# Optimization experiments

Hardware: AMD Instinct MI355X
Metric: run time of the kernel (lower is better)

Reference implementation:

```python
import jax, jax.numpy as jnp
import numpy as np

N_NODES = 50000
N_REL = 4
N_EDGES = 250000
IN_F, HID_F, OUT_F = 512, 512, 256


def setup_inputs() -> dict:
    key = jax.random.key(0)
    ks = jax.random.split(key, 9)
    x = jax.random.normal(ks[0], (N_NODES, IN_F), dtype=jnp.float32)
    edge_src = jax.random.randint(ks[1], (N_REL, N_EDGES), 0, N_NODES, dtype=jnp.int64)
    edge_dst = jax.random.randint(ks[2], (N_REL, N_EDGES), 0, N_NODES, dtype=jnp.int64)
    s1 = 1.0 / np.sqrt(IN_F)
    s2 = 1.0 / np.sqrt(HID_F)
    Wself1 = jax.random.normal(ks[3], (N_REL, IN_F, HID_F), dtype=jnp.float32) * s1
    Wneigh1 = jax.random.normal(ks[4], (N_REL, IN_F, HID_F), dtype=jnp.float32) * s1
    b1 = jnp.zeros((N_REL, HID_F), dtype=jnp.float32)
    Wself2 = jax.random.normal(ks[5], (N_REL, HID_F, OUT_F), dtype=jnp.float32) * s2
    Wneigh2 = jax.random.normal(ks[6], (N_REL, HID_F, OUT_F), dtype=jnp.float32) * s2
    b2 = jnp.zeros((N_REL, OUT_F), dtype=jnp.float32)
    return {"x": x, "Wself1": Wself1, "Wneigh1": Wneigh1, "b1": b1,
            "Wself2": Wself2, "Wneigh2": Wneigh2, "b2": b2,
            "edge_src": edge_src, "edge_dst": edge_dst}


def _hetero_sage_layer(h, Wself, Wneigh, b, edge_src, edge_dst):
    """HeteroGraphConv(sum) over per-relation SAGEConv(mean) layers.

    DGL SAGEConv(mean): out_r = h @ W_self_r + mean_in_neigh(h) @ W_neigh_r + b_r;
    zero-in-degree nodes get a zero neighbor term (divide by max(deg,1)).
    """
    n = h.shape[0]
    out = jnp.zeros((n, Wself.shape[-1]), dtype=h.dtype)
    for r in range(Wself.shape[0]):  # small fixed number of relations
        src, dst = edge_src[r], edge_dst[r]
        deg = jax.ops.segment_sum(jnp.ones(src.shape, dtype=h.dtype), dst, num_segments=n)
        neigh_sum = jax.ops.segment_sum(h[src], dst, num_segments=n)  # [n, d]
        neigh = neigh_sum / jnp.maximum(deg, 1.0)[:, None]
        out = out + h @ Wself[r] + neigh @ Wneigh[r] + b[r]
    return out


def reference(x, Wself1, Wneigh1, b1, Wself2, Wneigh2, b2, edge_src, edge_dst):
    h = _hetero_sage_layer(x, Wself1, Wneigh1, b1, edge_src, edge_dst)
    h = jax.nn.relu(h)
    return _hetero_sage_layer(h, Wself2, Wneigh2, b2, edge_src, edge_dst)
```

## Files before the change

kernel.cpp:

```cpp
#include <hip/hip_runtime.h>
#include <stdint.h>

#define NNODES 50000
#define NREL 4
#define NEDGES 250000
#define INF 512
#define HIDF 512
#define OUTF 256
#define KCAT 2560
#define SCANB 49

typedef unsigned short u16;
typedef u16 u16x8 __attribute__((ext_vector_type(8)));
typedef __bf16 bf16x8 __attribute__((ext_vector_type(8)));
typedef float f32x4 __attribute__((ext_vector_type(4)));

__device__ __forceinline__ float bf2f(u16 b) {
    unsigned u = ((unsigned)b) << 16;
    return __builtin_bit_cast(float, u);
}
__device__ __forceinline__ u16 f2bf(float f) {
    unsigned u = __builtin_bit_cast(unsigned, f);
    u = (u + 0x7fffu + ((u >> 16) & 1u)) >> 16;
    return (u16)u;
}

#define GLOAD_LDS16(gsrc, ldst)                                                  \
    __builtin_amdgcn_global_load_lds(                                            \
        (__attribute__((address_space(1))) void*)(gsrc),                         \
        (__attribute__((address_space(3))) void*)(ldst), 16, 0, 0)


__global__ void cast_bf16_kernel(const float* __restrict__ in, u16* __restrict__ out, long total) {
    long i = ((long)blockIdx.x * blockDim.x + threadIdx.x) * 8;
    long stride = (long)gridDim.x * blockDim.x * 8;
    for (; i + 7 < total; i += stride) {
        float4 v0 = *(const float4*)(in + i);
        float4 v1 = *(const float4*)(in + i + 4);
        u16x8 o;
        o[0] = f2bf(v0.x); o[1] = f2bf(v0.y); o[2] = f2bf(v0.z); o[3] = f2bf(v0.w);
        o[4] = f2bf(v1.x); o[5] = f2bf(v1.y); o[6] = f2bf(v1.z); o[7] = f2bf(v1.w);
        *(u16x8*)(out + i) = o;
    }
}

__global__ __launch_bounds__(256) void prep_w_kernel(
    const float* __restrict__ Ws1, const float* __restrict__ Wn1,
    const float* __restrict__ Ws2, const float* __restrict__ Wn2,
    u16* __restrict__ WT1, u16* __restrict__ WT2) {
    __shared__ float tile[64][65];
    int bid = blockIdx.x;
    const float* Wself; const float* Wneigh; u16* WT;
    int N, s, kt, nt;
    if (bid < 320) {
        N = HIDF; WT = WT1; Wself = Ws1; Wneigh = Wn1;
        s = bid >> 6; int r = bid & 63; kt = r >> 3; nt = r & 7;
    } else {
        int b = bid - 320;
        N = OUTF; WT = WT2; Wself = Ws2; Wneigh = Wn2;
        s = b >> 5; int r = b & 31; kt = r >> 2; nt = r & 3;
    }
    int l = threadIdx.x & 63, wv = threadIdx.x >> 6;
    int n0 = nt * 64 + l;
    for (int i = 0; i < 16; ++i) {
        int kl = wv + i * 4;
        int k = kt * 64 + kl;
        float v;
        if (s == 0) {
            v = Wself[(size_t)k * N + n0] + Wself[((size_t)512 + k) * N + n0] +
                Wself[((size_t)1024 + k) * N + n0] + Wself[((size_t)1536 + k) * N + n0];
        } else {
            v = Wneigh[((size_t)(s - 1) * 512 + k) * N + n0];
        }
        tile[kl][l] = v;
    }
    __syncthreads();
    for (int i = 0; i < 16; ++i) {
        int nl = wv + i * 4;
        WT[(size_t)(nt * 64 + nl) * KCAT + s * 512 + kt * 64 + l] = f2bf(tile[l][nl]);
    }
}

__global__ void prep_bias_kernel(const float* __restrict__ b1, const float* __restrict__ b2,
                                 float* __restrict__ b1s, float* __restrict__ b2s) {
    int t = threadIdx.x;
    if (t < HIDF) b1s[t] = b1[t] + b1[HIDF + t] + b1[2 * HIDF + t] + b1[3 * HIDF + t];
    if (t < OUTF) b2s[t] = b2[t] + b2[OUTF + t] + b2[2 * OUTF + t] + b2[3 * OUTF + t];
}


__global__ void hist_kernel(const int* __restrict__ dst, int* __restrict__ deg) {
    int r = blockIdx.y;
    int i = blockIdx.x * blockDim.x + threadIdx.x;
    if (i < NEDGES) atomicAdd(&deg[r * NNODES + dst[r * NEDGES + i]], 1);
}

__global__ __launch_bounds__(1024) void scan1_kernel(const int* __restrict__ deg,
                                                     int* __restrict__ rp, int* __restrict__ bsum) {
    int rel = blockIdx.x / SCANB, blk = blockIdx.x % SCANB;
    int i = blk * 1024 + threadIdx.x;
    int v = (i < NNODES) ? deg[rel * NNODES + i] : 0;
    __shared__ int wsum[16];
    int lane = threadIdx.x & 63, wid = threadIdx.x >> 6;
    int x = v;
#pragma unroll
    for (int off = 1; off < 64; off <<= 1) {
        int o = __shfl_up(x, off);
        if (lane >= off) x += o;
    }
    if (lane == 63) wsum[wid] = x;
    __syncthreads();
    if (wid == 0) {
        int s = (lane < 16) ? wsum[lane] : 0;
#pragma unroll
        for (int off = 1; off < 16; off <<= 1) {
            int o = __shfl_up(s, off);
            if (lane >= off) s += o;
        }
        if (lane < 16) wsum[lane] = s;
    }
    __syncthreads();
    int excl = (wid > 0 ? wsum[wid - 1] : 0) + x - v;
    if (i < NNODES) rp[rel * (NNODES + 1) + i] = excl;
    if (threadIdx.x == 1023) bsum[blockIdx.x] = excl + v;
}

__global__ void scan2_kernel(const int* __restrict__ bsum, int* __restrict__ bofs) {
    int r = threadIdx.x >> 6, lane = threadIdx.x & 63;
    int v = (lane < SCANB) ? bsum[r * SCANB + lane] : 0;
    int x = v;
#pragma unroll
    for (int off = 1; off < 64; off <<= 1) {
        int o = __shfl_up(x, off);
        if (lane >= off) x += o;
    }
    if (lane < SCANB) bofs[r * SCANB + lane] = x - v;
}

__global__ __launch_bounds__(1024) void scan3_kernel(int* __restrict__ rp, int* __restrict__ cur,
                                                     const int* __restrict__ bofs) {
    int rel = blockIdx.x / SCANB, blk = blockIdx.x % SCANB;
    int i = blk * 1024 + threadIdx.x;
    if (i < NNODES) {
        int v = rp[rel * (NNODES + 1) + i] + bofs[rel * SCANB + blk];
        rp[rel * (NNODES + 1) + i] = v;
        cur[rel * NNODES + i] = v;
        if (i == 0) rp[rel * (NNODES + 1) + NNODES] = NEDGES;
    }
}

__global__ void fill_kernel(const int* __restrict__ esrc, const int* __restrict__ edst,
                            int* __restrict__ cur, int* __restrict__ col) {
    int r = blockIdx.y;
    int i = blockIdx.x * blockDim.x + threadIdx.x;
    if (i < NEDGES) {
        int d = edst[r * NEDGES + i];
        int pos = atomicAdd(&cur[r * NNODES + d], 1);
        col[r * NEDGES + pos] = esrc[r * NEDGES + i];
    }
}


__global__ __launch_bounds__(256) void aggregate_kernel(const u16* __restrict__ src,
                                                        const int* __restrict__ rp,
                                                        const int* __restrict__ col,
                                                        u16* __restrict__ out) {
    int node = blockIdx.x * 4 + (threadIdx.x >> 6);
    int rel = blockIdx.y;
    if (node >= NNODES) return;
    const int* r = rp + rel * (NNODES + 1);
    const int* cl = col + rel * NEDGES;
    int l = threadIdx.x & 63;
    int p0 = r[node], p1 = r[node + 1];
    int d = p1 - p0;
    float scale = (d > 0) ? 1.0f / (float)d : 1.0f;
    float acc[8] = {0.f, 0.f, 0.f, 0.f, 0.f, 0.f, 0.f, 0.f};
    const u16* srcl = src + l * 8;
    for (int base = 0; base < d; base += 64) {
        int ci = p0 + base + l;
        int myc = cl[ci < p1 ? ci : (p1 - 1)];
        int lim = d - base;
        if (lim > 64) lim = 64;
        for (int e = 0; e < lim; e += 8) {
            int idx[8]; float wgt[8];
#pragma unroll
            for (int j = 0; j < 8; ++j) {
                int ee = e + j;
                int lane = (ee < lim) ? ee : e;
                idx[j] = __builtin_amdgcn_readlane(myc, lane);
                wgt[j] = (ee < lim) ? scale : 0.0f;
            }
            u16x8 v[8];
#pragma unroll
            for (int j = 0; j < 8; ++j) v[j] = *(const u16x8*)(srcl + (size_t)idx[j] * 512);
#pragma unroll
            for (int j = 0; j < 8; ++j)
#pragma unroll
                for (int f = 0; f < 8; ++f) acc[f] += wgt[j] * bf2f(v[j][f]);
        }
    }
    u16x8 o;
#pragma unroll
    for (int j = 0; j < 8; ++j) o[j] = f2bf(acc[j]);
    *(u16x8*)(out + ((size_t)rel * NNODES + node) * 512 + l * 8) = o;
}


template <int N, int OUTMODE>
__global__ __launch_bounds__(256, 4) void gemm_kernel(
    const u16* __restrict__ A0, const u16* __restrict__ A1, const u16* __restrict__ A2,
    const u16* __restrict__ A3, const u16* __restrict__ A4, const u16* __restrict__ WT,
    const float* __restrict__ bias, void* __restrict__ outp, int M) {
    __shared__ u16 ldsA[128 * 64];
    __shared__ u16 ldsB[128 * 64];
    const int t = threadIdx.x;
    const int w = t >> 6, l = t & 63;
    const int wr = w >> 1, wc = w & 1;

    constexpr int ncol = N >> 7;
    const int nwg = gridDim.x * gridDim.y;
    const int orig = blockIdx.y * gridDim.x + blockIdx.x;
    const int q = nwg >> 3, rr = nwg & 7, xcd = orig & 7, loc = orig >> 3;
    const int v = (xcd < rr) ? xcd * (q + 1) + loc : rr * (q + 1) + (xcd - rr) * q + loc;
    const int rowBase = (v / ncol) * 128;
    const int colBase = (v % ncol) * 128;

    f32x4 acc[4][4] = {};

    const u16* const As[5] = {A0, A1, A2, A3, A4};
    const int sr = t >> 3;
    const int gp = t & 7;
    const int lr = l & 15, lg = l >> 4;

#pragma unroll
    for (int s = 0; s < 5; ++s) {
        const u16* __restrict__ Asrc = As[s];
        for (int ts = 0; ts < 8; ++ts) {
            const int klocal = ts * 64;
            const int kglob = s * 512 + klocal;
#pragma unroll
            for (int c = 0; c < 4; ++c) {
                int r = c * 32 + sr;
                int gl = gp ^ (r & 7);
                int grow = rowBase + r;
                if (grow > M - 1) grow = M - 1;
                const u16* gsrc = Asrc + (size_t)grow * 512 + klocal + gl * 8;
                GLOAD_LDS16(gsrc, ldsA + (c * 2048 + w * 512));
            }
#pragma unroll
            for (int c = 0; c < 4; ++c) {
                int r = c * 32 + sr;
                int gl = gp ^ (r & 7);
                const u16* gsrc = WT + (size_t)(colBase + r) * KCAT + kglob + gl * 8;
                GLOAD_LDS16(gsrc, ldsB + (c * 2048 + w * 512));
            }
            __syncthreads();
#pragma unroll
            for (int kh = 0; kh < 2; ++kh) {
                bf16x8 av[4], bv[4];
#pragma unroll
                for (int m = 0; m < 4; ++m) {
                    int r = wr * 64 + m * 16 + lr;
                    int g = (kh * 4 + lg) ^ (r & 7);
                    av[m] = *(const bf16x8*)((const char*)ldsA + r * 128 + g * 16);
                }
#pragma unroll
                for (int n = 0; n < 4; ++n) {
                    int r = wc * 64 + n * 16 + lr;
                    int g = (kh * 4 + lg) ^ (r & 7);
                    bv[n] = *(const bf16x8*)((const char*)ldsB + r * 128 + g * 16);
                }
#pragma unroll
                for (int m = 0; m < 4; ++m)
#pragma unroll
                    for (int n = 0; n < 4; ++n)
                        acc[m][n] =
                            __builtin_amdgcn_mfma_f32_16x16x32_bf16(av[m], bv[n], acc[m][n], 0, 0, 0);
            }
            __syncthreads();
        }
    }

    const int lq = l >> 4;
#pragma unroll
    for (int m = 0; m < 4; ++m) {
#pragma unroll
        for (int n = 0; n < 4; ++n) {
#pragma unroll
            for (int j = 0; j < 4; ++j) {
                int row = rowBase + wr * 64 + m * 16 + lq * 4 + j;
                int colc = colBase + wc * 64 + n * 16 + lr;
                if (row < M) {
                    float vv = acc[m][n][j] + bias[colc];
                    if (OUTMODE == 0) {
                        vv = vv > 0.f ? vv : 0.f;
                        ((u16*)outp)[(size_t)row * N + colc] = f2bf(vv);
                    } else {
                        ((float*)outp)[(size_t)row * N + colc] = vv;
                    }
                }
            }
        }
    }
}


extern "C" void kernel_launch(void* const* d_in, const int* in_sizes, int n_in,
                              void* d_out, int out_size, void* d_ws, size_t ws_size,
                              hipStream_t stream) {
    const float* x = (const float*)d_in[0];
    const float* Wself1 = (const float*)d_in[1];
    const float* Wneigh1 = (const float*)d_in[2];
    const float* b1 = (const float*)d_in[3];
    const float* Wself2 = (const float*)d_in[4];
    const float* Wneigh2 = (const float*)d_in[5];
    const float* b2 = (const float*)d_in[6];
    const int* esrc = (const int*)d_in[7];
    const int* edst = (const int*)d_in[8];

    char* ws = (char*)d_ws;
    size_t off = 0;
    auto alloc = [&](size_t bytes) {
        char* p = ws + off;
        off += (bytes + 255) & ~(size_t)255;
        return p;
    };
    const size_t plane = (size_t)NNODES * 512;
    u16* xB = (u16*)alloc(plane * 2);
    u16* mB = (u16*)alloc(NREL * plane * 2);
    u16* h1B = (u16*)alloc(plane * 2);
    u16* WT1 = (u16*)alloc((size_t)HIDF * KCAT * 2);
    u16* WT2 = (u16*)alloc((size_t)OUTF * KCAT * 2);
    float* b1s = (float*)alloc(HIDF * 4);
    float* b2s = (float*)alloc(OUTF * 4);
    int* deg = (int*)alloc((size_t)NREL * NNODES * 4);
    int* rp = (int*)alloc((size_t)NREL * (NNODES + 1) * 4);
    int* cur = (int*)alloc((size_t)NREL * NNODES * 4);
    int* col = (int*)alloc((size_t)NREL * NEDGES * 4);
    int* bsum = (int*)alloc((size_t)NREL * SCANB * 4);
    int* bofs = (int*)alloc((size_t)NREL * SCANB * 4);

    hipMemsetAsync(deg, 0, (size_t)NREL * NNODES * 4, stream);
    cast_bf16_kernel<<<12500, 256, 0, stream>>>(x, xB, (long)NNODES * INF);
    prep_w_kernel<<<480, 256, 0, stream>>>(Wself1, Wneigh1, Wself2, Wneigh2, WT1, WT2);
    prep_bias_kernel<<<1, 512, 0, stream>>>(b1, b2, b1s, b2s);
    hist_kernel<<<dim3(977, 4), 256, 0, stream>>>(edst, deg);
    scan1_kernel<<<NREL * SCANB, 1024, 0, stream>>>(deg, rp, bsum);
    scan2_kernel<<<1, 256, 0, stream>>>(bsum, bofs);
    scan3_kernel<<<NREL * SCANB, 1024, 0, stream>>>(rp, cur, bofs);
    fill_kernel<<<dim3(977, 4), 256, 0, stream>>>(esrc, edst, cur, col);

    aggregate_kernel<<<dim3(12500, 4), 256, 0, stream>>>(xB, rp, col, mB);
    gemm_kernel<HIDF, 0><<<dim3(4, 391), 256, 0, stream>>>(
        xB, mB, mB + plane, mB + 2 * plane, mB + 3 * plane, WT1, b1s, h1B, NNODES);

    aggregate_kernel<<<dim3(12500, 4), 256, 0, stream>>>(h1B, rp, col, mB);
    gemm_kernel<OUTF, 1><<<dim3(2, 391), 256, 0, stream>>>(
        h1B, mB, mB + plane, mB + 2 * plane, mB + 3 * plane, WT2, b2s, d_out, NNODES);
}
```

Before: 843.4 us.

## Reorder layer-2 to transform-then-aggregate with a single projection GEMM

Layer 2 now runs one GEMM of h1 against a concatenated weight matrix with 1280 output columns (the summed self weight plus the four per-relation neighbor weights), writing a bf16 projection buffer P. A new aggregation kernel then gathers 256-wide projected neighbor rows per relation and adds them to the self term, writing fp32 output directly. This exploits linearity, mean(h)W = mean(hW), so the gather works on 256-wide rows instead of 512-wide ones and the GEMM's reduction dimension drops from 2560 to 512. In exchange the intermediate P is rounded to bf16 before accumulation, which adds extra rounding error to the final output.

```diff
diff --git a/kernel.cpp b/kernel.cpp
--- a/kernel.cpp
+++ b/kernel.cpp
@@ -3,14 +3,16 @@
 
 #define NNODES 50000
 #define NREL 4
-#define NEDGES 250000
 #define INF 512
 #define HIDF 512
 #define OUTF 256
+#define NEDGES 250000
 #define KCAT 2560
+#define N2 1280
 #define SCANB 49
 
 typedef unsigned short u16;
+typedef u16 u16x4 __attribute__((ext_vector_type(4)));
 typedef u16 u16x8 __attribute__((ext_vector_type(8)));
 typedef __bf16 bf16x8 __attribute__((ext_vector_type(8)));
 typedef float f32x4 __attribute__((ext_vector_type(4)));
@@ -50,42 +52,59 @@
     u16* __restrict__ WT1, u16* __restrict__ WT2) {
     __shared__ float tile[64][65];
     int bid = blockIdx.x;
-    const float* Wself; const float* Wneigh; u16* WT;
-    int N, s, kt, nt;
+    int l = threadIdx.x & 63, wv = threadIdx.x >> 6;
     if (bid < 320) {
-        N = HIDF; WT = WT1; Wself = Ws1; Wneigh = Wn1;
-        s = bid >> 6; int r = bid & 63; kt = r >> 3; nt = r & 7;
+        int s = bid >> 6, r = bid & 63, kt = r >> 3, nt = r & 7;
+        int n0 = nt * 64 + l;
+        for (int i = 0; i < 16; ++i) {
+            int kl = wv + i * 4;
+            int k = kt * 64 + kl;
+            float v;
+            if (s == 0) {
+                v = Ws1[(size_t)k * HIDF + n0] + Ws1[((size_t)512 + k) * HIDF + n0] +
+                    Ws1[((size_t)1024 + k) * HIDF + n0] + Ws1[((size_t)1536 + k) * HIDF + n0];
+            } else {
+                v = Wn1[((size_t)(s - 1) * 512 + k) * HIDF + n0];
+            }
+            tile[kl][l] = v;
+        }
+        __syncthreads();
+        for (int i = 0; i < 16; ++i) {
+            int nl = wv + i * 4;
+            WT1[(size_t)(nt * 64 + nl) * KCAT + s * 512 + kt * 64 + l] = f2bf(tile[l][nl]);
+        }
     } else {
         int b = bid - 320;
-        N = OUTF; WT = WT2; Wself = Ws2; Wneigh = Wn2;
-        s = b >> 5; int r = b & 31; kt = r >> 2; nt = r & 3;
-    }
-    int l = threadIdx.x & 63, wv = threadIdx.x >> 6;
-    int n0 = nt * 64 + l;
-    for (int i = 0; i < 16; ++i) {
-        int kl = wv + i * 4;
-        int k = kt * 64 + kl;
-        float v;
-        if (s == 0) {
-            v = Wself[(size_t)k * N + n0] + Wself[((size_t)512 + k) * N + n0] +
-                Wself[((size_t)1024 + k) * N + n0] + Wself[((size_t)1536 + k) * N + n0];
-        } else {
-            v = Wneigh[((size_t)(s - 1) * 512 + k) * N + n0];
-        }
-        tile[kl][l] = v;
-    }
-    __syncthreads();
-    for (int i = 0; i < 16; ++i) {
-        int nl = wv + i * 4;
-        WT[(size_t)(nt * 64 + nl) * KCAT + s * 512 + kt * 64 + l] = f2bf(tile[l][nl]);
+        int nt = b >> 3, kt = b & 7;
+        int n0 = nt * 64 + l;
+        int s = n0 >> 8, nn = n0 & 255;
+        for (int i = 0; i < 16; ++i) {
+            int kl = wv + i * 4;
+            int k = kt * 64 + kl;
+            float v;
+            if (s == 0) {
+                v = Ws2[(size_t)k * OUTF + nn] + Ws2[((size_t)512 + k) * OUTF + nn] +
+                    Ws2[((size_t)1024 + k) * OUTF + nn] + Ws2[((size_t)1536 + k) * OUTF + nn];
+            } else {
+                v = Wn2[((size_t)(s - 1) * 512 + k) * OUTF + nn];
+            }
+            tile[kl][l] = v;
+        }
+        __syncthreads();
+        for (int i = 0; i < 16; ++i) {
+            int nl = wv + i * 4;
+            WT2[(size_t)(nt * 64 + nl) * 512 + kt * 64 + l] = f2bf(tile[l][nl]);
+        }
     }
 }
 
 __global__ void prep_bias_kernel(const float* __restrict__ b1, const float* __restrict__ b2,
-                                 float* __restrict__ b1s, float* __restrict__ b2s) {
-    int t = threadIdx.x;
+                                 float* __restrict__ b1s, float* __restrict__ b2e) {
+    int t = blockIdx.x * 1024 + threadIdx.x;
     if (t < HIDF) b1s[t] = b1[t] + b1[HIDF + t] + b1[2 * HIDF + t] + b1[3 * HIDF + t];
-    if (t < OUTF) b2s[t] = b2[t] + b2[OUTF + t] + b2[2 * OUTF + t] + b2[3 * OUTF + t];
+    int i = t - 512;
+    if (i >= 0 && i < N2)
+        b2e[i] = (i < OUTF) ? (b2[i] + b2[OUTF + i] + b2[2 * OUTF + i] + b2[3 * OUTF + i]) : 0.f;
 }
 
 
@@ -206,7 +225,57 @@
 }
 
 
-template <int N, int OUTMODE>
+__global__ __launch_bounds__(256) void aggregate2_kernel(const u16* __restrict__ P,
+                                                         const int* __restrict__ rp,
+                                                         const int* __restrict__ col,
+                                                         float* __restrict__ out) {
+    int node = blockIdx.x * 4 + (threadIdx.x >> 6);
+    if (node >= NNODES) return;
+    int l = threadIdx.x & 63;
+    u16x4 sv = *(const u16x4*)(P + (size_t)node * N2 + l * 4);
+    float a0 = bf2f(sv[0]), a1 = bf2f(sv[1]), a2 = bf2f(sv[2]), a3 = bf2f(sv[3]);
+#pragma unroll
+    for (int r = 0; r < NREL; ++r) {
+        const int* rpn = rp + r * (NNODES + 1);
+        const int* cl = col + r * NEDGES;
+        int p0 = rpn[node], p1 = rpn[node + 1];
+        int d = p1 - p0;
+        if (d <= 0) continue;
+        float scale = 1.0f / (float)d;
+        const u16* base = P + 256 + r * 256 + (size_t)l * 4;
+        for (int b = 0; b < d; b += 64) {
+            int ci = p0 + b + l;
+            int myc = cl[ci < p1 ? ci : (p1 - 1)];
+            int lim = d - b;
+            if (lim > 64) lim = 64;
+            for (int e = 0; e < lim; e += 8) {
+                int idx[8]; float wgt[8];
+#pragma unroll
+                for (int j = 0; j < 8; ++j) {
+                    int ee = e + j;
+                    idx[j] = __builtin_amdgcn_readlane(myc, (ee < lim) ? ee : e);
+                    wgt[j] = (ee < lim) ? scale : 0.0f;
+                }
+                u16x4 v[8];
+#pragma unroll
+                for (int j = 0; j < 8; ++j)
+                    v[j] = *(const u16x4*)(base + (size_t)idx[j] * N2);
+#pragma unroll
+                for (int j = 0; j < 8; ++j) {
+                    a0 += wgt[j] * bf2f(v[j][0]);
+                    a1 += wgt[j] * bf2f(v[j][1]);
+                    a2 += wgt[j] * bf2f(v[j][2]);
+                    a3 += wgt[j] * bf2f(v[j][3]);
+                }
+            }
+        }
+    }
+    float4 o = {a0, a1, a2, a3};
+    *(float4*)(out + (size_t)node * OUTF + l * 4) = o;
+}
+
+
+template <int N, int NPL, int OUTMODE>
 __global__ __launch_bounds__(256, 4) void gemm_kernel(
     const u16* __restrict__ A0, const u16* __restrict__ A1, const u16* __restrict__ A2,
     const u16* __restrict__ A3, const u16* __restrict__ A4, const u16* __restrict__ WT,
@@ -216,6 +285,7 @@
     const int t = threadIdx.x;
     const int w = t >> 6, l = t & 63;
     const int wr = w >> 1, wc = w & 1;
+    constexpr int KTOT = NPL * 512;
 
     constexpr int ncol = N >> 7;
     const int nwg = gridDim.x * gridDim.y;
@@ -233,7 +303,7 @@
     const int lr = l & 15, lg = l >> 4;
 
 #pragma unroll
-    for (int s = 0; s < 5; ++s) {
+    for (int s = 0; s < NPL; ++s) {
         const u16* __restrict__ Asrc = As[s];
         for (int ts = 0; ts < 8; ++ts) {
             const int klocal = ts * 64;
@@ -251,7 +321,7 @@
             for (int c = 0; c < 4; ++c) {
                 int r = c * 32 + sr;
                 int gl = gp ^ (r & 7);
-                const u16* gsrc = WT + (size_t)(colBase + r) * KCAT + kglob + gl * 8;
+                const u16* gsrc = WT + (size_t)(colBase + r) * KTOT + kglob + gl * 8;
                 GLOAD_LDS16(gsrc, ldsB + (c * 2048 + w * 512));
             }
             __syncthreads();
@@ -292,12 +362,8 @@
                 int colc = colBase + wc * 64 + n * 16 + lr;
                 if (row < M) {
                     float vv = acc[m][n][j] + bias[colc];
-                    if (OUTMODE == 0) {
-                        vv = vv > 0.f ? vv : 0.f;
-                        ((u16*)outp)[(size_t)row * N + colc] = f2bf(vv);
-                    } else {
-                        ((float*)outp)[(size_t)row * N + colc] = vv;
-                    }
+                    if (OUTMODE == 0) vv = vv > 0.f ? vv : 0.f;
+                    ((u16*)outp)[(size_t)row * N + colc] = f2bf(vv);
                 }
             }
         }
@@ -330,9 +396,9 @@
     u16* mB = (u16*)alloc(NREL * plane * 2);
     u16* h1B = (u16*)alloc(plane * 2);
     u16* WT1 = (u16*)alloc((size_t)HIDF * KCAT * 2);
-    u16* WT2 = (u16*)alloc((size_t)OUTF * KCAT * 2);
+    u16* WT2 = (u16*)alloc((size_t)N2 * 512 * 2);
     float* b1s = (float*)alloc(HIDF * 4);
-    float* b2s = (float*)alloc(OUTF * 4);
+    float* b2e = (float*)alloc(N2 * 4);
     int* deg = (int*)alloc((size_t)NREL * NNODES * 4);
     int* rp = (int*)alloc((size_t)NREL * (NNODES + 1) * 4);
     int* cur = (int*)alloc((size_t)NREL * NNODES * 4);
@@ -343,7 +409,7 @@
     hipMemsetAsync(deg, 0, (size_t)NREL * NNODES * 4, stream);
     cast_bf16_kernel<<<12500, 256, 0, stream>>>(x, xB, (long)NNODES * INF);
     prep_w_kernel<<<480, 256, 0, stream>>>(Wself1, Wneigh1, Wself2, Wneigh2, WT1, WT2);
-    prep_bias_kernel<<<1, 512, 0, stream>>>(b1, b2, b1s, b2s);
+    prep_bias_kernel<<<2, 1024, 0, stream>>>(b1, b2, b1s, b2e);
     hist_kernel<<<dim3(977, 4), 256, 0, stream>>>(edst, deg);
     scan1_kernel<<<NREL * SCANB, 1024, 0, stream>>>(deg, rp, bsum);
     scan2_kernel<<<1, 256, 0, stream>>>(bsum, bofs);
@@ -351,10 +417,11 @@
     fill_kernel<<<dim3(977, 4), 256, 0, stream>>>(esrc, edst, cur, col);
 
     aggregate_kernel<<<dim3(12500, 4), 256, 0, stream>>>(xB, rp, col, mB);
-    gemm_kernel<HIDF, 0><<<dim3(4, 391), 256, 0, stream>>>(
+    gemm_kernel<HIDF, 5, 0><<<dim3(4, 391), 256, 0, stream>>>(
         xB, mB, mB + plane, mB + 2 * plane, mB + 3 * plane, WT1, b1s, h1B, NNODES);
 
-    aggregate_kernel<<<dim3(12500, 4), 256, 0, stream>>>(h1B, rp, col, mB);
-    gemm_kernel<OUTF, 1><<<dim3(2, 391), 256, 0, stream>>>(
-        h1B, mB, mB + plane, mB + 2 * plane, mB + 3 * plane, WT2, b2s, d_out, NNODES);
-}
+    u16* P = mB;
+    gemm_kernel<N2, 1, 2><<<dim3(10, 391), 256, 0, stream>>>(
+        h1B, h1B, h1B, h1B, h1B, WT2, b2e, P, NNODES);
+    aggregate2_kernel<<<12500, 256, 0, stream>>>(P, rp, col, (float*)d_out);
+}
```

After: 795.9 us. 5.6% less time.
